# Optimization experiments

Measured on AMD Instinct MI355X. Metric: run time of the kernel, lower is better.

## Reference

```python
import jax, jax.numpy as jnp
import numpy as np


def setup_inputs() -> dict:
    key = jax.random.key(0)
    ks = jax.random.split(key, 10)
    N, E = 50000, 1600000
    IN, H, OUT = 32, 64, 16
    x = jax.random.normal(ks[0], (N, IN), dtype=jnp.float32)
    edge_index = jax.random.randint(ks[1], (2, E), 0, N, dtype=jnp.int64)
    edge_attr = jax.random.normal(ks[2], (E, 3), dtype=jnp.float32)
    s1 = 1.0 / np.sqrt(2 * IN + 3)
    W1 = jax.random.uniform(ks[3], (2 * IN + 3, H), jnp.float32, -s1, s1)
    b1 = jax.random.uniform(ks[4], (H,), jnp.float32, -s1, s1)
    s2 = 1.0 / np.sqrt(H)
    W2 = jax.random.uniform(ks[5], (H, H), jnp.float32, -s2, s2)
    b2 = jax.random.uniform(ks[6], (H,), jnp.float32, -s2, s2)
    Wo = jax.random.uniform(ks[7], (H, OUT), jnp.float32, -s2, s2)
    bo = jax.random.uniform(ks[8], (OUT,), jnp.float32, -s2, s2)
    return {"x": x, "edge_index": edge_index, "edge_attr": edge_attr,
            "W1": W1, "b1": b1, "W2": W2, "b2": b2, "Wo": Wo, "bo": bo}


def reference(x, edge_index, edge_attr, W1, b1, W2, b2, Wo, bo):
    N = x.shape[0]
    src, dst = edge_index[0], edge_index[1]  # PyG: x_j = x[src], x_i = x[dst]
    x_i = x[dst]                      # [E, IN]
    x_j = x[src]                      # [E, IN]
    tmp = jnp.concatenate([x_i, x_j - x_i, edge_attr], axis=1)  # [E, 2*IN+3]
    h = jax.nn.relu(tmp @ W1 + b1)    # [E, H]
    msg = h @ W2 + b2                 # [E, H]
    # max-aggregate messages to destination nodes; empty segments -> 0 (PyG fill)
    agg = jax.ops.segment_max(msg, dst, num_segments=N)
    agg = jnp.where(jnp.isfinite(agg), agg, 0.0)
    out = jax.nn.sigmoid(agg @ Wo + bo)  # [N, OUT]
    return out
```

## Files before the change

### kernel.cpp

```cpp
#include <hip/hip_runtime.h>

#define IN_F 32
#define HID 64
#define OUTF 16
#define NSUB 8
#define SB_CAP 16
#define OVF_CAP 65536
#define ORD_NEG_INF 0x007FFFFFu

typedef _Float16 v8h __attribute__((ext_vector_type(8)));
typedef float v4f __attribute__((ext_vector_type(4)));

__device__ __forceinline__ unsigned ordenc(float v) {
  unsigned b = __float_as_uint(v);
  return (b & 0x80000000u) ? ~b : (b | 0x80000000u);
}
__device__ __forceinline__ float orddec(unsigned u) {
  unsigned b = (u & 0x80000000u) ? (u & 0x7FFFFFFFu) : ~u;
  return __uint_as_float(b);
}
__device__ __forceinline__ unsigned short f2h_bits(float f) {
  _Float16 h = (_Float16)f; unsigned short u; __builtin_memcpy(&u, &h, 2); return u;
}
__device__ __forceinline__ float h_bits2f(unsigned short u) {
  _Float16 h; __builtin_memcpy(&h, &u, 2); return (float)h;
}

__global__ __launch_bounds__(256) void node_pre_kernel(
    const float* __restrict__ x, const float* __restrict__ W1,
    const float* __restrict__ b1, float* __restrict__ P, float* __restrict__ Q, int N)
{
  const int lane = threadIdx.x & 63;
  float w1d[IN_F], w1b[IN_F];
#pragma unroll
  for (int c = 0; c < IN_F; ++c) {
    w1b[c] = W1[(IN_F + c) * HID + lane];
    w1d[c] = W1[c * HID + lane] - w1b[c];
  }
  const float b1v = b1[lane];
  int gw = __builtin_amdgcn_readfirstlane((blockIdx.x << 2) | (threadIdx.x >> 6));
  const int nwaves = gridDim.x << 2;
  for (int n = gw; n < N; n += nwaves) {
    float p = b1v, q = 0.f;
#pragma unroll
    for (int c = 0; c < IN_F; ++c) {
      float xv = x[n * IN_F + c];
      p = fmaf(xv, w1d[c], p);
      q = fmaf(xv, w1b[c], q);
    }
    P[n * HID + lane] = p;
    Q[n * HID + lane] = q;
  }
}

__global__ __launch_bounds__(256) void scatter_kernel(
    const int* __restrict__ ei, const float* __restrict__ ea,
    uint2* __restrict__ rec, int* __restrict__ cnt,
    int* __restrict__ ovf, int* __restrict__ ovf_cnt, int E)
{
  int e = blockIdx.x * 256 + threadIdx.x;
  if (e >= E) return;
  int s = ei[e];
  int d = ei[(size_t)E + e];
  float a0 = ea[e * 3 + 0], a1 = ea[e * 3 + 1], a2 = ea[e * 3 + 2];
  int g = blockIdx.x & (NSUB - 1);
  int sb = d * NSUB + g;
  int pos = atomicAdd(&cnt[sb], 1);
  if (pos < SB_CAP) {
    uint2 r;
    r.x = (unsigned)s | ((unsigned)f2h_bits(a0) << 16);
    r.y = (unsigned)f2h_bits(a1) | ((unsigned)f2h_bits(a2) << 16);
    rec[(size_t)sb * SB_CAP + pos] = r;
  } else {
    int oi = atomicAdd(ovf_cnt, 1);
    if (oi < OVF_CAP) ovf[oi] = e;
  }
}

__global__ __launch_bounds__(256) void bucket_kernel(
    const uint2* __restrict__ rec, const int* __restrict__ cnt,
    const float* __restrict__ W1, const float* __restrict__ W2,
    const float* __restrict__ P, const float* __restrict__ Q,
    unsigned* __restrict__ agg, int N)
{
  __shared__ __align__(16) _Float16 hB[4][16][72];
  __shared__ uint2 stage[4][NSUB * SB_CAP];
  __shared__ unsigned rowS[4][HID];

  const int wave = threadIdx.x >> 6;
  const int lane = threadIdx.x & 63;
  const int quad = lane >> 4;
  const int eidx = lane & 15;

  v8h a_frag[4][2];
#pragma unroll
  for (int t = 0; t < 4; ++t)
#pragma unroll
    for (int ks = 0; ks < 2; ++ks)
#pragma unroll
      for (int j = 0; j < 8; ++j)
        a_frag[t][ks][j] = (_Float16)W2[(ks * 32 + quad * 8 + j) * HID + t * 16 + eidx];

  const float w1c0 = W1[(2 * IN_F + 0) * HID + lane];
  const float w1c1 = W1[(2 * IN_F + 1) * HID + lane];
  const float w1c2 = W1[(2 * IN_F + 2) * HID + lane];

  const int gwave = __builtin_amdgcn_readfirstlane((blockIdx.x << 2) | wave);
  const int nw = gridDim.x << 2;

  for (int d = gwave; d < N; d += nw) {
    const uint4 ca = *(const uint4*)&cnt[(size_t)d * NSUB];
    const uint4 cb = *(const uint4*)&cnt[(size_t)d * NSUB + 4];
    int c0 = min((int)ca.x, SB_CAP), c1 = min((int)ca.y, SB_CAP);
    int c2 = min((int)ca.z, SB_CAP), c3 = min((int)ca.w, SB_CAP);
    int c4 = min((int)cb.x, SB_CAP), c5 = min((int)cb.y, SB_CAP);
    int c6 = min((int)cb.z, SB_CAP), c7 = min((int)cb.w, SB_CAP);
    int p1 = c0, p2 = p1 + c1, p3 = p2 + c2, p4 = p3 + c3;
    int p5 = p4 + c4, p6 = p5 + c5, p7 = p6 + c6;
    const int m = p7 + c7;

    if (m == 0) { agg[(size_t)d * HID + lane] = ORD_NEG_INF; continue; }

#pragma unroll
    for (int rr = 0; rr < 2; ++rr) {
      int i = rr * 64 + lane;
      if (i < m) {
        int g = 0, base = 0;
        if (i >= p1) { g = 1; base = p1; }
        if (i >= p2) { g = 2; base = p2; }
        if (i >= p3) { g = 3; base = p3; }
        if (i >= p4) { g = 4; base = p4; }
        if (i >= p5) { g = 5; base = p5; }
        if (i >= p6) { g = 6; base = p6; }
        if (i >= p7) { g = 7; base = p7; }
        stage[wave][i] = rec[((size_t)d * NSUB + g) * SB_CAP + (i - base)];
      }
    }
    __builtin_amdgcn_wave_barrier();

    const float pvl = P[(size_t)d * HID + lane];
    float maxv[4][4];
#pragma unroll
    for (int t = 0; t < 4; ++t)
#pragma unroll
      for (int r = 0; r < 4; ++r) maxv[t][r] = -INFINITY;

    const int ntile = (m + 15) >> 4;
    float qv[16];
#pragma unroll
    for (int i = 0; i < 16; ++i) {
      int idx = min(i, m - 1);
      uint2 r = stage[wave][idx];
      qv[i] = Q[(size_t)(r.x & 0xFFFFu) * HID + lane];
    }

    for (int tb = 0; tb < ntile; ++tb) {
#pragma unroll
      for (int i = 0; i < 16; ++i) {
        int idx = min(tb * 16 + i, m - 1);
        uint2 r = stage[wave][idx];
        float pre = pvl + qv[i];
        pre = fmaf(h_bits2f((unsigned short)(r.x >> 16)), w1c0, pre);
        pre = fmaf(h_bits2f((unsigned short)(r.y & 0xFFFFu)), w1c1, pre);
        pre = fmaf(h_bits2f((unsigned short)(r.y >> 16)), w1c2, pre);
        hB[wave][i][lane] = (_Float16)fmaxf(pre, 0.f);
      }
      if (tb + 1 < ntile) {
#pragma unroll
        for (int i = 0; i < 16; ++i) {
          int idx = min((tb + 1) * 16 + i, m - 1);
          uint2 r = stage[wave][idx];
          qv[i] = Q[(size_t)(r.x & 0xFFFFu) * HID + lane];
        }
      }
      __builtin_amdgcn_wave_barrier();

      const v8h bf0 = *(const v8h*)&hB[wave][eidx][quad * 8];
      const v8h bf1 = *(const v8h*)&hB[wave][eidx][32 + quad * 8];
#pragma unroll
      for (int t = 0; t < 4; ++t) {
        v4f acc = (v4f){0.f, 0.f, 0.f, 0.f};
        acc = __builtin_amdgcn_mfma_f32_16x16x32_f16(a_frag[t][0], bf0, acc, 0, 0, 0);
        acc = __builtin_amdgcn_mfma_f32_16x16x32_f16(a_frag[t][1], bf1, acc, 0, 0, 0);
#pragma unroll
        for (int r = 0; r < 4; ++r) maxv[t][r] = fmaxf(maxv[t][r], acc[r]);
      }
      __builtin_amdgcn_wave_barrier();
    }

#pragma unroll
    for (int t = 0; t < 4; ++t)
#pragma unroll
      for (int r = 0; r < 4; ++r) {
        float v = maxv[t][r];
        v = fmaxf(v, __shfl_xor(v, 1, 64));
        v = fmaxf(v, __shfl_xor(v, 2, 64));
        v = fmaxf(v, __shfl_xor(v, 4, 64));
        v = fmaxf(v, __shfl_xor(v, 8, 64));
        maxv[t][r] = v;
      }
    float val = maxv[0][0];
#pragma unroll
    for (int t = 0; t < 4; ++t)
#pragma unroll
      for (int r = 0; r < 4; ++r)
        val = (eidx == t * 4 + r) ? maxv[t][r] : val;
    rowS[wave][((eidx >> 2) << 4) + (quad << 2) + (eidx & 3)] = ordenc(val);
    __builtin_amdgcn_wave_barrier();
    agg[(size_t)d * HID + lane] = rowS[wave][lane];
    __builtin_amdgcn_wave_barrier();
  }
}

__global__ __launch_bounds__(256) void overflow_kernel(
    const int* __restrict__ ei, const float* __restrict__ ea,
    const float* __restrict__ W1, const float* __restrict__ W2,
    const float* __restrict__ P, const float* __restrict__ Q,
    const int* __restrict__ ovf, const int* __restrict__ ovf_cnt,
    unsigned* __restrict__ agg, int E)
{
  __shared__ float hsh[4][HID];
  const int wave = threadIdx.x >> 6;
  const int lane = threadIdx.x & 63;

  int M = *ovf_cnt;
  if (M > OVF_CAP) M = OVF_CAP;
  if (M == 0) return;

  float w2r[HID];
#pragma unroll
  for (int j = 0; j < HID; ++j) w2r[j] = W2[j * HID + lane];
  const float w1c0 = W1[(2 * IN_F + 0) * HID + lane];
  const float w1c1 = W1[(2 * IN_F + 1) * HID + lane];
  const float w1c2 = W1[(2 * IN_F + 2) * HID + lane];

  const int gwave = __builtin_amdgcn_readfirstlane((blockIdx.x << 2) | wave);
  const int nw = gridDim.x << 2;
  for (int k = gwave; k < M; k += nw) {
    int e = ovf[k];
    int s = ei[e];
    int d = ei[(size_t)E + e];
    float pre = P[(size_t)d * HID + lane] + Q[(size_t)s * HID + lane];
    pre = fmaf(ea[e * 3 + 0], w1c0, pre);
    pre = fmaf(ea[e * 3 + 1], w1c1, pre);
    pre = fmaf(ea[e * 3 + 2], w1c2, pre);
    hsh[wave][lane] = fmaxf(pre, 0.f);
    __builtin_amdgcn_wave_barrier();
    float mv = 0.f;
#pragma unroll
    for (int j = 0; j < HID; ++j) mv = fmaf(hsh[wave][j], w2r[j], mv);
    atomicMax(&agg[(size_t)d * HID + lane], ordenc(mv));
    __builtin_amdgcn_wave_barrier();
  }
}

__global__ __launch_bounds__(256) void out_kernel(
    const unsigned* __restrict__ agg,
    const float* __restrict__ b2,
    const float* __restrict__ Wo, const float* __restrict__ bo,
    float* __restrict__ out, int N)
{
  __shared__ float Wos[HID * OUTF];
  __shared__ float bos[OUTF];
  __shared__ float b2s[HID];
  __shared__ float aggs[16][HID + 1];

  for (int i = threadIdx.x; i < HID * OUTF; i += 256) Wos[i] = Wo[i];
  if (threadIdx.x < OUTF) bos[threadIdx.x] = bo[threadIdx.x];
  if (threadIdx.x < HID) b2s[threadIdx.x] = b2[threadIdx.x];
  __syncthreads();

  const int nodeBase = blockIdx.x * 16;
  {
    int ln = threadIdx.x >> 4;
    int k0 = (threadIdx.x & 15) * 4;
    int n = nodeBase + ln;
    if (n < N) {
      const uint4 u = *(const uint4*)&agg[n * HID + k0];
      aggs[ln][k0 + 0] = (u.x == ORD_NEG_INF) ? 0.f : orddec(u.x) + b2s[k0 + 0];
      aggs[ln][k0 + 1] = (u.y == ORD_NEG_INF) ? 0.f : orddec(u.y) + b2s[k0 + 1];
      aggs[ln][k0 + 2] = (u.z == ORD_NEG_INF) ? 0.f : orddec(u.z) + b2s[k0 + 2];
      aggs[ln][k0 + 3] = (u.w == ORD_NEG_INF) ? 0.f : orddec(u.w) + b2s[k0 + 3];
    }
  }
  __syncthreads();
  {
    int ln = threadIdx.x >> 4;
    int o = threadIdx.x & 15;
    int n = nodeBase + ln;
    if (n < N) {
      float acc = bos[o];
#pragma unroll
      for (int k = 0; k < HID; ++k) acc = fmaf(aggs[ln][k], Wos[k * OUTF + o], acc);
      out[n * OUTF + o] = 1.f / (1.f + __expf(-acc));
    }
  }
}

extern "C" void kernel_launch(void* const* d_in, const int* in_sizes, int n_in,
                              void* d_out, int out_size, void* d_ws, size_t ws_size,
                              hipStream_t stream) {
  const float* x  = (const float*)d_in[0];
  const int*   ei = (const int*)d_in[1];
  const float* ea = (const float*)d_in[2];
  const float* W1 = (const float*)d_in[3];
  const float* b1 = (const float*)d_in[4];
  const float* W2 = (const float*)d_in[5];
  const float* b2 = (const float*)d_in[6];
  const float* Wo = (const float*)d_in[7];
  const float* bo = (const float*)d_in[8];
  float* out = (float*)d_out;

  const int N = in_sizes[0] / IN_F;
  const int E = in_sizes[1] / 2;

  char* w = (char*)d_ws;
  float*    Pp  = (float*)w;                     w += (size_t)N * HID * 4;
  float*    Qp  = (float*)w;                     w += (size_t)N * HID * 4;
  unsigned* agg = (unsigned*)w;                  w += (size_t)N * HID * 4;
  uint2*    rec = (uint2*)w;                     w += (size_t)N * NSUB * SB_CAP * 8;
  int*      cnt = (int*)w;                       w += (size_t)N * NSUB * 4;
  int*  ovf_cnt = (int*)w;                       w += 16;
  int*      ovf = (int*)w;

  hipMemsetAsync(cnt, 0, (size_t)N * NSUB * 4 + 16, stream);

  node_pre_kernel<<<512, 256, 0, stream>>>(x, W1, b1, Pp, Qp, N);
  scatter_kernel<<<(E + 255) / 256, 256, 0, stream>>>(ei, ea, rec, cnt, ovf, ovf_cnt, E);
  bucket_kernel<<<2048, 256, 0, stream>>>(rec, cnt, W1, W2, Pp, Qp, agg, N);
  overflow_kernel<<<256, 256, 0, stream>>>(ei, ea, W1, W2, Pp, Qp, ovf, ovf_cnt, agg, E);
  out_kernel<<<(N + 15) / 16, 256, 0, stream>>>(agg, b2, Wo, bo, out, N);
}
```

Measured before the change: 296.2 us.

## Fuse node precompute with edge scatter and prefetch next node's bucket

Merges the node pre-projection and edge scatter kernels into one launch, with scatter blocks each handling 1024 edges and batching their atomics. The bucket kernel now loads the next destination's counts, records and P row into registers while the current node is being computed, and stages them in double-buffered shared memory. It also writes the aggregate straight from the permuted lane index instead of going through a shared-memory transpose, and doubles the bucket grid. The aim is to cut launch overhead and hide gather latency, at the cost of more register pressure and a changed sub-bucket grouping (blockIdx&7 now spans 1024-edge blocks).

Result: no change. 292.4 us (-1.3%).

```diff
diff --git a/kernel.cpp b/kernel.cpp
--- a/kernel.cpp
+++ b/kernel.cpp
@@ -26,10 +26,53 @@
   _Float16 h; __builtin_memcpy(&h, &u, 2); return (float)h;
 }
 
-__global__ __launch_bounds__(256) void node_pre_kernel(
-    const float* __restrict__ x, const float* __restrict__ W1,
-    const float* __restrict__ b1, float* __restrict__ P, float* __restrict__ Q, int N)
+__global__ __launch_bounds__(256) void pre_scatter_kernel(
+    const float* __restrict__ x, const int* __restrict__ ei,
+    const float* __restrict__ ea, const float* __restrict__ W1,
+    const float* __restrict__ b1,
+    float* __restrict__ P, float* __restrict__ Q,
+    uint2* __restrict__ rec, int* __restrict__ cnt,
+    int* __restrict__ ovf, int* __restrict__ ovf_cnt,
+    int E, int N, int nSB)
 {
+  if (blockIdx.x < (unsigned)nSB) {
+    const int t = threadIdx.x;
+    const int base = blockIdx.x * 1024;
+    const int g = blockIdx.x & (NSUB - 1);
+    int e[4], s[4], d[4], pos[4];
+    bool v[4];
+#pragma unroll
+    for (int i = 0; i < 4; ++i) {
+      e[i] = base + i * 256 + t;
+      v[i] = e[i] < E;
+      int ec = v[i] ? e[i] : 0;
+      s[i] = ei[ec];
+      d[i] = ei[(size_t)E + ec];
+    }
+#pragma unroll
+    for (int i = 0; i < 4; ++i)
+      pos[i] = v[i] ? atomicAdd(&cnt[d[i] * NSUB + g], 1) : SB_CAP;
+    float a0[4], a1[4], a2[4];
+#pragma unroll
+    for (int i = 0; i < 4; ++i) {
+      int ec = v[i] ? e[i] : 0;
+      a0[i] = ea[ec * 3 + 0]; a1[i] = ea[ec * 3 + 1]; a2[i] = ea[ec * 3 + 2];
+    }
+#pragma unroll
+    for (int i = 0; i < 4; ++i) {
+      if (!v[i]) continue;
+      if (pos[i] < SB_CAP) {
+        uint2 r;
+        r.x = (unsigned)s[i] | ((unsigned)f2h_bits(a0[i]) << 16);
+        r.y = (unsigned)f2h_bits(a1[i]) | ((unsigned)f2h_bits(a2[i]) << 16);
+        rec[((size_t)d[i] * NSUB + g) * SB_CAP + pos[i]] = r;
+      } else {
+        int oi = atomicAdd(ovf_cnt, 1);
+        if (oi < OVF_CAP) ovf[oi] = e[i];
+      }
+    }
+    return;
+  }
   const int lane = threadIdx.x & 63;
   float w1d[IN_F], w1b[IN_F];
 #pragma unroll
@@ -38,8 +81,8 @@
     w1d[c] = W1[c * HID + lane] - w1b[c];
   }
   const float b1v = b1[lane];
-  int gw = __builtin_amdgcn_readfirstlane((blockIdx.x << 2) | (threadIdx.x >> 6));
-  const int nwaves = gridDim.x << 2;
+  int gw = __builtin_amdgcn_readfirstlane((((int)blockIdx.x - nSB) << 2) | (threadIdx.x >> 6));
+  const int nwaves = 512 << 2;
   for (int n = gw; n < N; n += nwaves) {
     float p = b1v, q = 0.f;
 #pragma unroll
@@ -50,30 +93,6 @@
     }
     P[n * HID + lane] = p;
     Q[n * HID + lane] = q;
-  }
-}
-
-__global__ __launch_bounds__(256) void scatter_kernel(
-    const int* __restrict__ ei, const float* __restrict__ ea,
-    uint2* __restrict__ rec, int* __restrict__ cnt,
-    int* __restrict__ ovf, int* __restrict__ ovf_cnt, int E)
-{
-  int e = blockIdx.x * 256 + threadIdx.x;
-  if (e >= E) return;
-  int s = ei[e];
-  int d = ei[(size_t)E + e];
-  float a0 = ea[e * 3 + 0], a1 = ea[e * 3 + 1], a2 = ea[e * 3 + 2];
-  int g = blockIdx.x & (NSUB - 1);
-  int sb = d * NSUB + g;
-  int pos = atomicAdd(&cnt[sb], 1);
-  if (pos < SB_CAP) {
-    uint2 r;
-    r.x = (unsigned)s | ((unsigned)f2h_bits(a0) << 16);
-    r.y = (unsigned)f2h_bits(a1) | ((unsigned)f2h_bits(a2) << 16);
-    rec[(size_t)sb * SB_CAP + pos] = r;
-  } else {
-    int oi = atomicAdd(ovf_cnt, 1);
-    if (oi < OVF_CAP) ovf[oi] = e;
   }
 }
 
@@ -84,13 +103,13 @@
     unsigned* __restrict__ agg, int N)
 {
   __shared__ __align__(16) _Float16 hB[4][16][72];
-  __shared__ uint2 stage[4][NSUB * SB_CAP];
-  __shared__ unsigned rowS[4][HID];
+  __shared__ uint2 stage[4][2][NSUB * SB_CAP];
 
   const int wave = threadIdx.x >> 6;
   const int lane = threadIdx.x & 63;
   const int quad = lane >> 4;
   const int eidx = lane & 15;
+  const int mych = ((eidx >> 2) << 4) + (quad << 2) + (eidx & 3);
 
   v8h a_frag[4][2];
 #pragma unroll
@@ -108,7 +127,11 @@
   const int gwave = __builtin_amdgcn_readfirstlane((blockIdx.x << 2) | wave);
   const int nw = gridDim.x << 2;
 
-  for (int d = gwave; d < N; d += nw) {
+  int d = gwave;
+  if (d >= N) return;
+
+  int m; uint2 r0, r1; float pP;
+  {
     const uint4 ca = *(const uint4*)&cnt[(size_t)d * NSUB];
     const uint4 cb = *(const uint4*)&cnt[(size_t)d * NSUB + 4];
     int c0 = min((int)ca.x, SB_CAP), c1 = min((int)ca.y, SB_CAP);
@@ -117,10 +140,7 @@
     int c6 = min((int)cb.z, SB_CAP), c7 = min((int)cb.w, SB_CAP);
     int p1 = c0, p2 = p1 + c1, p3 = p2 + c2, p4 = p3 + c3;
     int p5 = p4 + c4, p6 = p5 + c5, p7 = p6 + c6;
-    const int m = p7 + c7;
-
-    if (m == 0) { agg[(size_t)d * HID + lane] = ORD_NEG_INF; continue; }
-
+    m = p7 + c7;
 #pragma unroll
     for (int rr = 0; rr < 2; ++rr) {
       int i = rr * 64 + lane;
@@ -133,82 +153,152 @@
         if (i >= p5) { g = 5; base = p5; }
         if (i >= p6) { g = 6; base = p6; }
         if (i >= p7) { g = 7; base = p7; }
-        stage[wave][i] = rec[((size_t)d * NSUB + g) * SB_CAP + (i - base)];
-      }
-    }
+        uint2 rv = rec[((size_t)d * NSUB + g) * SB_CAP + (i - base)];
+        if (rr == 0) r0 = rv; else r1 = rv;
+      }
+    }
+    pP = P[(size_t)d * HID + lane];
+  }
+
+  int cur = 0;
+  while (d < N) {
+    const int dn = d + nw;
+    const int m_cur = m;
+    const float pvl = pP;
+
+    if (lane < m_cur) stage[wave][cur][lane] = r0;
+    if (64 + lane < m_cur) stage[wave][cur][64 + lane] = r1;
     __builtin_amdgcn_wave_barrier();
 
-    const float pvl = P[(size_t)d * HID + lane];
-    float maxv[4][4];
-#pragma unroll
-    for (int t = 0; t < 4; ++t)
-#pragma unroll
-      for (int r = 0; r < 4; ++r) maxv[t][r] = -INFINITY;
-
-    const int ntile = (m + 15) >> 4;
-    float qv[16];
-#pragma unroll
-    for (int i = 0; i < 16; ++i) {
-      int idx = min(i, m - 1);
-      uint2 r = stage[wave][idx];
-      qv[i] = Q[(size_t)(r.x & 0xFFFFu) * HID + lane];
-    }
-
-    for (int tb = 0; tb < ntile; ++tb) {
+    if (m_cur > 0) {
+      float qv[16];
 #pragma unroll
       for (int i = 0; i < 16; ++i) {
-        int idx = min(tb * 16 + i, m - 1);
-        uint2 r = stage[wave][idx];
-        float pre = pvl + qv[i];
-        pre = fmaf(h_bits2f((unsigned short)(r.x >> 16)), w1c0, pre);
-        pre = fmaf(h_bits2f((unsigned short)(r.y & 0xFFFFu)), w1c1, pre);
-        pre = fmaf(h_bits2f((unsigned short)(r.y >> 16)), w1c2, pre);
-        hB[wave][i][lane] = (_Float16)fmaxf(pre, 0.f);
-      }
-      if (tb + 1 < ntile) {
+        int idx = min(i, m_cur - 1);
+        uint2 rr = stage[wave][cur][idx];
+        qv[i] = Q[(size_t)(rr.x & 0xFFFFu) * HID + lane];
+      }
+
+      if (dn < N) {
+        const uint4 ca = *(const uint4*)&cnt[(size_t)dn * NSUB];
+        const uint4 cb = *(const uint4*)&cnt[(size_t)dn * NSUB + 4];
+        int c0 = min((int)ca.x, SB_CAP), c1 = min((int)ca.y, SB_CAP);
+        int c2 = min((int)ca.z, SB_CAP), c3 = min((int)ca.w, SB_CAP);
+        int c4 = min((int)cb.x, SB_CAP), c5 = min((int)cb.y, SB_CAP);
+        int c6 = min((int)cb.z, SB_CAP), c7 = min((int)cb.w, SB_CAP);
+        int p1 = c0, p2 = p1 + c1, p3 = p2 + c2, p4 = p3 + c3;
+        int p5 = p4 + c4, p6 = p5 + c5, p7 = p6 + c6;
+        m = p7 + c7;
+#pragma unroll
+        for (int rr = 0; rr < 2; ++rr) {
+          int i = rr * 64 + lane;
+          if (i < m) {
+            int g = 0, base = 0;
+            if (i >= p1) { g = 1; base = p1; }
+            if (i >= p2) { g = 2; base = p2; }
+            if (i >= p3) { g = 3; base = p3; }
+            if (i >= p4) { g = 4; base = p4; }
+            if (i >= p5) { g = 5; base = p5; }
+            if (i >= p6) { g = 6; base = p6; }
+            if (i >= p7) { g = 7; base = p7; }
+            uint2 rv = rec[((size_t)dn * NSUB + g) * SB_CAP + (i - base)];
+            if (rr == 0) r0 = rv; else r1 = rv;
+          }
+        }
+        pP = P[(size_t)dn * HID + lane];
+      }
+
+      float maxv[4][4];
+#pragma unroll
+      for (int t = 0; t < 4; ++t)
+#pragma unroll
+        for (int r = 0; r < 4; ++r) maxv[t][r] = -INFINITY;
+
+      const int ntile = (m_cur + 15) >> 4;
+      for (int tb = 0; tb < ntile; ++tb) {
 #pragma unroll
         for (int i = 0; i < 16; ++i) {
-          int idx = min((tb + 1) * 16 + i, m - 1);
-          uint2 r = stage[wave][idx];
-          qv[i] = Q[(size_t)(r.x & 0xFFFFu) * HID + lane];
-        }
-      }
-      __builtin_amdgcn_wave_barrier();
-
-      const v8h bf0 = *(const v8h*)&hB[wave][eidx][quad * 8];
-      const v8h bf1 = *(const v8h*)&hB[wave][eidx][32 + quad * 8];
-#pragma unroll
-      for (int t = 0; t < 4; ++t) {
-        v4f acc = (v4f){0.f, 0.f, 0.f, 0.f};
-        acc = __builtin_amdgcn_mfma_f32_16x16x32_f16(a_frag[t][0], bf0, acc, 0, 0, 0);
-        acc = __builtin_amdgcn_mfma_f32_16x16x32_f16(a_frag[t][1], bf1, acc, 0, 0, 0);
-#pragma unroll
-        for (int r = 0; r < 4; ++r) maxv[t][r] = fmaxf(maxv[t][r], acc[r]);
-      }
-      __builtin_amdgcn_wave_barrier();
-    }
-
-#pragma unroll
-    for (int t = 0; t < 4; ++t)
-#pragma unroll
-      for (int r = 0; r < 4; ++r) {
-        float v = maxv[t][r];
-        v = fmaxf(v, __shfl_xor(v, 1, 64));
-        v = fmaxf(v, __shfl_xor(v, 2, 64));
-        v = fmaxf(v, __shfl_xor(v, 4, 64));
-        v = fmaxf(v, __shfl_xor(v, 8, 64));
-        maxv[t][r] = v;
-      }
-    float val = maxv[0][0];
-#pragma unroll
-    for (int t = 0; t < 4; ++t)
-#pragma unroll
-      for (int r = 0; r < 4; ++r)
-        val = (eidx == t * 4 + r) ? maxv[t][r] : val;
-    rowS[wave][((eidx >> 2) << 4) + (quad << 2) + (eidx & 3)] = ordenc(val);
-    __builtin_amdgcn_wave_barrier();
-    agg[(size_t)d * HID + lane] = rowS[wave][lane];
-    __builtin_amdgcn_wave_barrier();
+          int idx = min(tb * 16 + i, m_cur - 1);
+          uint2 rr = stage[wave][cur][idx];
+          float pre = pvl + qv[i];
+          pre = fmaf(h_bits2f((unsigned short)(rr.x >> 16)), w1c0, pre);
+          pre = fmaf(h_bits2f((unsigned short)(rr.y & 0xFFFFu)), w1c1, pre);
+          pre = fmaf(h_bits2f((unsigned short)(rr.y >> 16)), w1c2, pre);
+          hB[wave][i][lane] = (_Float16)fmaxf(pre, 0.f);
+        }
+        if (tb + 1 < ntile) {
+#pragma unroll
+          for (int i = 0; i < 16; ++i) {
+            int idx = min((tb + 1) * 16 + i, m_cur - 1);
+            uint2 rr = stage[wave][cur][idx];
+            qv[i] = Q[(size_t)(rr.x & 0xFFFFu) * HID + lane];
+          }
+        }
+        __builtin_amdgcn_wave_barrier();
+
+        const v8h bf0 = *(const v8h*)&hB[wave][eidx][quad * 8];
+        const v8h bf1 = *(const v8h*)&hB[wave][eidx][32 + quad * 8];
+#pragma unroll
+        for (int t = 0; t < 4; ++t) {
+          v4f acc = (v4f){0.f, 0.f, 0.f, 0.f};
+          acc = __builtin_amdgcn_mfma_f32_16x16x32_f16(a_frag[t][0], bf0, acc, 0, 0, 0);
+          acc = __builtin_amdgcn_mfma_f32_16x16x32_f16(a_frag[t][1], bf1, acc, 0, 0, 0);
+#pragma unroll
+          for (int r = 0; r < 4; ++r) maxv[t][r] = fmaxf(maxv[t][r], acc[r]);
+        }
+        __builtin_amdgcn_wave_barrier();
+      }
+
+#pragma unroll
+      for (int t = 0; t < 4; ++t)
+#pragma unroll
+        for (int r = 0; r < 4; ++r) {
+          float v = maxv[t][r];
+          v = fmaxf(v, __shfl_xor(v, 1, 64));
+          v = fmaxf(v, __shfl_xor(v, 2, 64));
+          v = fmaxf(v, __shfl_xor(v, 4, 64));
+          v = fmaxf(v, __shfl_xor(v, 8, 64));
+          maxv[t][r] = v;
+        }
+      float val = maxv[0][0];
+#pragma unroll
+      for (int t = 0; t < 4; ++t)
+#pragma unroll
+        for (int r = 0; r < 4; ++r)
+          val = (eidx == t * 4 + r) ? maxv[t][r] : val;
+      agg[(size_t)d * HID + mych] = ordenc(val);
+    } else {
+      if (dn < N) {
+        const uint4 ca = *(const uint4*)&cnt[(size_t)dn * NSUB];
+        const uint4 cb = *(const uint4*)&cnt[(size_t)dn * NSUB + 4];
+        int c0 = min((int)ca.x, SB_CAP), c1 = min((int)ca.y, SB_CAP);
+        int c2 = min((int)ca.z, SB_CAP), c3 = min((int)ca.w, SB_CAP);
+        int c4 = min((int)cb.x, SB_CAP), c5 = min((int)cb.y, SB_CAP);
+        int c6 = min((int)cb.z, SB_CAP), c7 = min((int)cb.w, SB_CAP);
+        int p1 = c0, p2 = p1 + c1, p3 = p2 + c2, p4 = p3 + c3;
+        int p5 = p4 + c4, p6 = p5 + c5, p7 = p6 + c6;
+        m = p7 + c7;
+#pragma unroll
+        for (int rr = 0; rr < 2; ++rr) {
+          int i = rr * 64 + lane;
+          if (i < m) {
+            int g = 0, base = 0;
+            if (i >= p1) { g = 1; base = p1; }
+            if (i >= p2) { g = 2; base = p2; }
+            if (i >= p3) { g = 3; base = p3; }
+            if (i >= p4) { g = 4; base = p4; }
+            if (i >= p5) { g = 5; base = p5; }
+            if (i >= p6) { g = 6; base = p6; }
+            if (i >= p7) { g = 7; base = p7; }
+            uint2 rv = rec[((size_t)dn * NSUB + g) * SB_CAP + (i - base)];
+            if (rr == 0) r0 = rv; else r1 = rv;
+          }
+        }
+        pP = P[(size_t)dn * HID + lane];
+      }
+      agg[(size_t)d * HID + lane] = ORD_NEG_INF;
+    }
+    d = dn; cur ^= 1;
   }
 }
 
@@ -325,9 +415,10 @@
 
   hipMemsetAsync(cnt, 0, (size_t)N * NSUB * 4 + 16, stream);
 
-  node_pre_kernel<<<512, 256, 0, stream>>>(x, W1, b1, Pp, Qp, N);
-  scatter_kernel<<<(E + 255) / 256, 256, 0, stream>>>(ei, ea, rec, cnt, ovf, ovf_cnt, E);
-  bucket_kernel<<<2048, 256, 0, stream>>>(rec, cnt, W1, W2, Pp, Qp, agg, N);
+  const int nSB = (E + 1023) / 1024;
+  pre_scatter_kernel<<<nSB + 512, 256, 0, stream>>>(
+      x, ei, ea, W1, b1, Pp, Qp, rec, cnt, ovf, ovf_cnt, E, N, nSB);
+  bucket_kernel<<<4096, 256, 0, stream>>>(rec, cnt, W1, W2, Pp, Qp, agg, N);
   overflow_kernel<<<256, 256, 0, stream>>>(ei, ea, W1, W2, Pp, Qp, ovf, ovf_cnt, agg, E);
   out_kernel<<<(N + 15) / 16, 256, 0, stream>>>(agg, b2, Wo, bo, out, N);
 }
```
